# Performance work log

Measured on AMD Instinct MI355X. Metric: run time of the kernel, lower is better.

## Reference

```python
import jax, jax.numpy as jnp
import numpy as np

N_NODES = 40000


def setup_inputs() -> dict:
    key = jax.random.key(0)
    k_h, k_w, k_b, k_s, k_d = jax.random.split(key, 5)
    in_feats, out_feats, n_edges = 128, 128, 640000
    h = jax.random.normal(k_h, (N_NODES, in_feats), dtype=jnp.float32)
    # nn.Linear(in_feats, out_feats): weight [out, in], bias [out]
    W = jax.random.normal(k_w, (out_feats, in_feats), dtype=jnp.float32) * (1.0 / np.sqrt(in_feats))
    b = jax.random.normal(k_b, (out_feats,), dtype=jnp.float32) * 0.01
    src = jax.random.randint(k_s, (n_edges,), 0, N_NODES, dtype=jnp.int32)
    dst = jax.random.randint(k_d, (n_edges,), 0, N_NODES, dtype=jnp.int32)
    return {"h": h, "W": W, "b": b, "src": src, "dst": dst}


def reference(h, W, b, src, dst):
    # update_all(copy_u('h','m'), sum('m','h_N')):
    # gather messages from source nodes, segment-sum into destination nodes.
    msgs = h[src]                                              # [E, in_feats] irregular gather
    agg = jax.ops.segment_sum(msgs, dst, num_segments=N_NODES)  # [N, in_feats] scatter-add
    # Source module applies the linear to h (agg is computed but unused there);
    # we return agg as a second output so the SpMM is observable.
    out = h @ W.T + b                                          # [N, out_feats]
    return out, agg
```

## Files before the change

kernel.cpp:

```cpp
#include <hip/hip_runtime.h>

#define FEAT   128
#define RS     64
#define RSH    6
#define CAPN   64
#define NRMAX  1024
#define PART   256
#define SLOTS  32
#define SLOTSH 5
#define STR    (PART * SLOTS)

typedef short bf16x8 __attribute__((ext_vector_type(8)));
typedef float f32x4  __attribute__((ext_vector_type(4)));

__device__ __forceinline__ unsigned pack_bf16x2(float x, float y) {
    unsigned ux = __float_as_uint(x);
    ux = (ux + 0x7fffu + ((ux >> 16) & 1u)) >> 16;
    unsigned uy = __float_as_uint(y);
    uy = (uy + 0x7fffu + ((uy >> 16) & 1u)) & 0xffff0000u;
    return uy | ux;
}

__device__ __forceinline__ bf16x8 pack8(float4 a, float4 b) {
    uint4 u = make_uint4(pack_bf16x2(a.x, a.y), pack_bf16x2(a.z, a.w),
                         pack_bf16x2(b.x, b.y), pack_bf16x2(b.z, b.w));
    return __builtin_bit_cast(bf16x8, u);
}

__device__ __forceinline__ f32x4 unpack2(unsigned x, unsigned y) {
    return (f32x4){__uint_as_float(x << 16), __uint_as_float(x & 0xffff0000u),
                   __uint_as_float(y << 16), __uint_as_float(y & 0xffff0000u)};
}

__global__ __launch_bounds__(512) void fused_kernel(
    const float* __restrict__ h, const float* __restrict__ W,
    const float* __restrict__ b, const int* __restrict__ src,
    const int* __restrict__ dst, float* __restrict__ out,
    uint4* __restrict__ hb4, unsigned* __restrict__ seg, int* __restrict__ cnt,
    int n, int E, int NR)
{
    __shared__ int hist[NRMAX];

    const int bid = blockIdx.x;
    const int tid = threadIdx.x;

    if (bid < PART) {
        for (int i = tid; i < NR; i += 512) hist[i] = 0;
        __syncthreads();

        const int epb = (((E + PART - 1) / PART) + 3) & ~3;
        const int e0  = bid * epb;
        int e1 = e0 + epb; if (e1 > E) e1 = E;

        if (e0 < e1) {
            const int nq4 = (e1 - e0) >> 2;
            const int4* __restrict__ d4p = (const int4*)(dst + e0);
            const int4* __restrict__ s4p = (const int4*)(src + e0);
            const size_t sb = (size_t)bid * SLOTS;

            for (int i = tid; i < nq4; i += 512) {
                int4 d = d4p[i];
                int4 s = s4p[i];
#pragma unroll
                for (int u = 0; u < 4; ++u) {
                    int dv = (u == 0) ? d.x : (u == 1) ? d.y : (u == 2) ? d.z : d.w;
                    int sv = (u == 0) ? s.x : (u == 1) ? s.y : (u == 2) ? s.z : s.w;
                    int rid  = dv >> RSH;
                    int slot = atomicAdd(&hist[rid], 1);
                    if (slot < SLOTS)
                        seg[(size_t)rid * STR + sb + slot] =
                            (unsigned)(((dv & (RS - 1)) << 16) | (sv & 0xffff));
                }
            }
            for (int e = e0 + (nq4 << 2) + tid; e < e1; e += 512) {
                int dv = dst[e], sv = src[e];
                int rid  = dv >> RSH;
                int slot = atomicAdd(&hist[rid], 1);
                if (slot < SLOTS)
                    seg[(size_t)rid * STR + sb + slot] =
                        (unsigned)(((dv & (RS - 1)) << 16) | (sv & 0xffff));
            }
        }
        __syncthreads();

        for (int r = tid; r < NR; r += 512) {
            int c = hist[r]; if (c > SLOTS) c = SLOTS;
            cnt[(size_t)r * PART + bid] = c;
        }
        return;
    }

    const int gbid = bid - PART;
    const int w    = tid >> 6;
    const int lane = tid & 63;
    const int m    = lane & 15, quad = lane >> 4;
    const int r0g  = gbid * 128 + (w >> 1) * 32;
    const int ch   = w & 1;
    if (r0g >= n) return;

    const float4* __restrict__ h4 = (const float4*)h;
    const float4* __restrict__ W4 = (const float4*)W;

    bf16x8 af[2][4];
#pragma unroll
    for (int mt = 0; mt < 2; ++mt) {
        int gr = r0g + mt * 16 + m;
#pragma unroll
        for (int ks = 0; ks < 4; ++ks) {
            float4 a0 = h4[(size_t)gr * 32 + ks * 8 + quad * 2];
            float4 a1 = h4[(size_t)gr * 32 + ks * 8 + quad * 2 + 1];
            af[mt][ks] = pack8(a0, a1);
        }
    }

    if (ch == 0) {
#pragma unroll
        for (int mt = 0; mt < 2; ++mt) {
            int gr = r0g + mt * 16 + m;
            if (gr < n) {
#pragma unroll
                for (int ks = 0; ks < 4; ++ks)
                    hb4[(size_t)gr * 16 + ks * 4 + quad] = __builtin_bit_cast(uint4, af[mt][ks]);
            }
        }
    }

    f32x4 acc[2][4];
#pragma unroll
    for (int mt = 0; mt < 2; ++mt)
#pragma unroll
        for (int nn = 0; nn < 4; ++nn) acc[mt][nn] = (f32x4){0.f, 0.f, 0.f, 0.f};

#pragma unroll
    for (int nn = 0; nn < 4; ++nn) {
        int c = (ch * 4 + nn) * 16 + m;
#pragma unroll
        for (int ks = 0; ks < 4; ++ks) {
            float4 b0 = W4[(size_t)c * 32 + ks * 8 + quad * 2];
            float4 b1 = W4[(size_t)c * 32 + ks * 8 + quad * 2 + 1];
            bf16x8 bf = pack8(b0, b1);
#pragma unroll
            for (int mt = 0; mt < 2; ++mt)
                acc[mt][nn] = __builtin_amdgcn_mfma_f32_16x16x32_bf16(
                    af[mt][ks], bf, acc[mt][nn], 0, 0, 0);
        }
    }

#pragma unroll
    for (int nn = 0; nn < 4; ++nn) {
        int col = (ch * 4 + nn) * 16 + m;
        float bias = b[col];
#pragma unroll
        for (int mt = 0; mt < 2; ++mt)
#pragma unroll
            for (int r = 0; r < 4; ++r) {
                int gr = r0g + mt * 16 + quad * 4 + r;
                if (gr < n)
                    __builtin_nontemporal_store(acc[mt][nn][r] + bias,
                                                &out[(size_t)gr * FEAT + col]);
            }
    }
}

__global__ __launch_bounds__(512) void bin_gather_kernel(
    const uint4* __restrict__ hb4, const unsigned* __restrict__ seg,
    const int* __restrict__ cnt, float* __restrict__ agg, int n, int NR)
{
    __shared__ int            lcnt[RS];
    __shared__ int            scnt[PART];
    __shared__ unsigned short lbkt[RS * CAPN];

    const int bid = blockIdx.x;
    const int tid = threadIdx.x;

    const int base = bid * RS;
    int rsv = n - base; if (rsv > RS) rsv = RS;

    if (tid < RS) lcnt[tid] = 0;
    if (tid < PART) scnt[tid] = cnt[(size_t)bid * PART + tid];
    __syncthreads();

    const int4* __restrict__ seg4 = (const int4*)seg + (size_t)bid * (STR / 4);
#pragma unroll
    for (int wv = 0; wv < STR / 4 / 512; ++wv) {
        int j4 = wv * 512 + tid;
        int4 pv = seg4[j4];
        int s0 = j4 << 2;
#pragma unroll
        for (int u = 0; u < 4; ++u) {
            int sl = s0 + u;
            unsigned p = (u == 0) ? (unsigned)pv.x : (u == 1) ? (unsigned)pv.y
                       : (u == 2) ? (unsigned)pv.z : (unsigned)pv.w;
            if ((sl & (SLOTS - 1)) < scnt[sl >> SLOTSH]) {
                int nd = (int)(p >> 16);
                int k  = atomicAdd(&lcnt[nd], 1);
                if (k < CAPN) lbkt[(nd << 6) + k] = (unsigned short)(p & 0xffffu);
            }
        }
    }
    __syncthreads();

    const int lane = tid & 63;
    const int w    = tid >> 6;
    const int q    = lane >> 4, ql = lane & 15;
    const int nb   = w << 3;

    for (int k = 0; k < 8; k += 2) {
        const int ndA = nb + k, ndB = nb + k + 1;
        if (ndA >= rsv) break;
        const bool hasB = (ndB < rsv);
        int degA = lcnt[ndA]; degA = degA > CAPN ? CAPN : degA;
        int degB = hasB ? lcnt[ndB] : 0; degB = degB > CAPN ? CAPN : degB;
        const int dmax = degA > degB ? degA : degB;
        const int rbA = ndA << 6, rbB = ndB << 6;

        f32x4 alA0 = {0.f,0.f,0.f,0.f}, ahA0 = {0.f,0.f,0.f,0.f};
        f32x4 alA1 = {0.f,0.f,0.f,0.f}, ahA1 = {0.f,0.f,0.f,0.f};
        f32x4 alB0 = {0.f,0.f,0.f,0.f}, ahB0 = {0.f,0.f,0.f,0.f};
        f32x4 alB1 = {0.f,0.f,0.f,0.f}, ahB1 = {0.f,0.f,0.f,0.f};

        for (int t = 0; t < dmax; t += 16) {
            const int i0 = t + q, i1 = t + 4 + q, i2 = t + 8 + q, i3 = t + 12 + q;
            int eA0 = lbkt[rbA + i0], eA1 = lbkt[rbA + i1];
            int eA2 = lbkt[rbA + i2], eA3 = lbkt[rbA + i3];
            int eB0 = lbkt[rbB + i0], eB1 = lbkt[rbB + i1];
            int eB2 = lbkt[rbB + i2], eB3 = lbkt[rbB + i3];
            uint4 vA0, vA1, vA2, vA3, vB0, vB1, vB2, vB3;
            if (i0 < degA) vA0 = hb4[(size_t)eA0 * 16 + ql];
            if (i1 < degA) vA1 = hb4[(size_t)eA1 * 16 + ql];
            if (i2 < degA) vA2 = hb4[(size_t)eA2 * 16 + ql];
            if (i3 < degA) vA3 = hb4[(size_t)eA3 * 16 + ql];
            if (i0 < degB) vB0 = hb4[(size_t)eB0 * 16 + ql];
            if (i1 < degB) vB1 = hb4[(size_t)eB1 * 16 + ql];
            if (i2 < degB) vB2 = hb4[(size_t)eB2 * 16 + ql];
            if (i3 < degB) vB3 = hb4[(size_t)eB3 * 16 + ql];
            if (i0 < degA) { alA0 += unpack2(vA0.x, vA0.y); ahA0 += unpack2(vA0.z, vA0.w); }
            if (i1 < degA) { alA1 += unpack2(vA1.x, vA1.y); ahA1 += unpack2(vA1.z, vA1.w); }
            if (i2 < degA) { alA0 += unpack2(vA2.x, vA2.y); ahA0 += unpack2(vA2.z, vA2.w); }
            if (i3 < degA) { alA1 += unpack2(vA3.x, vA3.y); ahA1 += unpack2(vA3.z, vA3.w); }
            if (i0 < degB) { alB0 += unpack2(vB0.x, vB0.y); ahB0 += unpack2(vB0.z, vB0.w); }
            if (i1 < degB) { alB1 += unpack2(vB1.x, vB1.y); ahB1 += unpack2(vB1.z, vB1.w); }
            if (i2 < degB) { alB0 += unpack2(vB2.x, vB2.y); ahB0 += unpack2(vB2.z, vB2.w); }
            if (i3 < degB) { alB1 += unpack2(vB3.x, vB3.y); ahB1 += unpack2(vB3.z, vB3.w); }
        }

        alA0 += alA1; ahA0 += ahA1;
        alB0 += alB1; ahB0 += ahB1;

#pragma unroll
        for (int j = 0; j < 4; ++j) {
            alA0[j] += __shfl_down(alA0[j], 32);
            ahA0[j] += __shfl_down(ahA0[j], 32);
            alB0[j] += __shfl_down(alB0[j], 32);
            ahB0[j] += __shfl_down(ahB0[j], 32);
            alA0[j] += __shfl_down(alA0[j], 16);
            ahA0[j] += __shfl_down(ahA0[j], 16);
            alB0[j] += __shfl_down(alB0[j], 16);
            ahB0[j] += __shfl_down(ahB0[j], 16);
        }

        if (q == 0) {
            f32x4* aggv = (f32x4*)agg;
            __builtin_nontemporal_store(alA0, &aggv[(size_t)(base + ndA) * 32 + ql * 2]);
            __builtin_nontemporal_store(ahA0, &aggv[(size_t)(base + ndA) * 32 + ql * 2 + 1]);
            if (hasB) {
                __builtin_nontemporal_store(alB0, &aggv[(size_t)(base + ndB) * 32 + ql * 2]);
                __builtin_nontemporal_store(ahB0, &aggv[(size_t)(base + ndB) * 32 + ql * 2 + 1]);
            }
        }
    }
}

__global__ __launch_bounds__(256, 2) void gemm_f32_kernel(
    const float* __restrict__ h, const float* __restrict__ W,
    const float* __restrict__ b, float* __restrict__ out, int nrows)
{
    __shared__ float4 wsh[128 * 8];
    __shared__ float4 hsh[64 * 8];
    const int tid = threadIdx.x;
    const int tx  = tid & 31;
    const int ty  = tid >> 5;
    const int r0  = blockIdx.x * 64;
    const float4* __restrict__ W4 = (const float4*)W;
    const float4* __restrict__ h4 = (const float4*)h;
    float acc[8][4];
#pragma unroll
    for (int i = 0; i < 8; ++i)
#pragma unroll
        for (int j = 0; j < 4; ++j) acc[i][j] = 0.f;
    for (int p = 0; p < 4; ++p) {
        if (p) __syncthreads();
#pragma unroll
        for (int l = 0; l < 4; ++l) {
            int flat = l * 256 + tid;
            int c = flat >> 3, kc = flat & 7;
            wsh[c * 8 + (kc ^ ((c >> 2) & 7))] = W4[c * 32 + p * 8 + kc];
        }
#pragma unroll
        for (int l = 0; l < 2; ++l) {
            int flat = l * 256 + tid;
            int r = flat >> 3, kc = flat & 7;
            int gr = r0 + r;
            float4 v = make_float4(0.f, 0.f, 0.f, 0.f);
            if (gr < nrows) v = h4[(size_t)gr * 32 + p * 8 + kc];
            hsh[r * 8 + (kc ^ ((r >> 2) & 7))] = v;
        }
        __syncthreads();
#pragma unroll
        for (int kc = 0; kc < 8; ++kc) {
            float4 wv[4], hv[8];
#pragma unroll
            for (int j = 0; j < 4; ++j) wv[j] = wsh[(4 * tx + j) * 8 + (kc ^ (tx & 7))];
#pragma unroll
            for (int i = 0; i < 8; ++i) {
                int r = 8 * ty + i;
                hv[i] = hsh[r * 8 + (kc ^ ((r >> 2) & 7))];
            }
#pragma unroll
            for (int i = 0; i < 8; ++i)
#pragma unroll
                for (int j = 0; j < 4; ++j) {
                    acc[i][j] += hv[i].x * wv[j].x;
                    acc[i][j] += hv[i].y * wv[j].y;
                    acc[i][j] += hv[i].z * wv[j].z;
                    acc[i][j] += hv[i].w * wv[j].w;
                }
        }
    }
    const float4 bj = ((const float4*)b)[tx];
    float4* out4 = (float4*)out;
#pragma unroll
    for (int i = 0; i < 8; ++i) {
        int gr = r0 + 8 * ty + i;
        if (gr < nrows) {
            float4 o;
            o.x = acc[i][0] + bj.x; o.y = acc[i][1] + bj.y;
            o.z = acc[i][2] + bj.z; o.w = acc[i][3] + bj.w;
            out4[(size_t)gr * 32 + tx] = o;
        }
    }
}

__global__ __launch_bounds__(256) void scatter_add_kernel(
    const float* __restrict__ h, const int* __restrict__ src,
    const int* __restrict__ dst, float* __restrict__ agg, int E)
{
    int gid  = blockIdx.x * 256 + threadIdx.x;
    int e    = gid >> 6;
    int lane = gid & 63;
    if (e >= E) return;
    int s = src[e];
    int d = dst[e];
    const float2* hp = (const float2*)(h + (size_t)s * FEAT);
    float2 v = hp[lane];
    float* ap = agg + (size_t)d * FEAT + 2 * lane;
    unsafeAtomicAdd(ap,     v.x);
    unsafeAtomicAdd(ap + 1, v.y);
}

extern "C" void kernel_launch(void* const* d_in, const int* in_sizes, int n_in,
                              void* d_out, int out_size, void* d_ws, size_t ws_size,
                              hipStream_t stream) {
    const float* h   = (const float*)d_in[0];
    const float* W   = (const float*)d_in[1];
    const float* b   = (const float*)d_in[2];
    const int*   src = (const int*)d_in[3];
    const int*   dst = (const int*)d_in[4];

    const int n = in_sizes[0] / FEAT;
    const int E = in_sizes[3];

    float* out = (float*)d_out;
    float* agg = out + (size_t)n * FEAT;

    const int NR = (n + RS - 1) >> RSH;

    size_t hb_bytes  = (size_t)n * FEAT * 2;
    size_t seg_bytes = (size_t)NR * STR * 4;
    size_t cnt_bytes = (size_t)NR * PART * 4;
    size_t need = hb_bytes + seg_bytes + cnt_bytes;

    bool fast = (ws_size >= need) && (n > 0) && (n <= 65536) && (NR <= NRMAX);

    if (fast) {
        uint4*    hb  = (uint4*)d_ws;
        unsigned* seg = (unsigned*)((char*)d_ws + hb_bytes);
        int*      cnt = (int*)((char*)d_ws + hb_bytes + seg_bytes);

        int gemm_blocks = (n + 127) / 128;
        fused_kernel<<<dim3(PART + gemm_blocks), dim3(512), 0, stream>>>(
            h, W, b, src, dst, out, hb, seg, cnt, n, E, NR);

        bin_gather_kernel<<<dim3(NR), dim3(512), 0, stream>>>(
            hb, seg, cnt, agg, n, NR);
    } else {
        gemm_f32_kernel<<<dim3((n + 63) / 64), dim3(256), 0, stream>>>(h, W, b, out, n);
        (void)hipMemsetAsync(agg, 0, (size_t)n * FEAT * sizeof(float), stream);
        int nblocks = (int)(((long long)E * 64 + 255) / 256);
        scatter_add_kernel<<<dim3(nblocks), dim3(256), 0, stream>>>(h, src, dst, agg, E);
    }
}
```

Measured before the change: 150.9 us.

## Split bf16 feature copy into feature planes and gather per plane

The bf16 copy of h is now stored as 8 feature planes of 16 values each (32 bytes per node per plane), so each plane is 1.25 MB instead of one 10 MB table. The binning and gather stages are split into two kernels: bin_kernel writes per-range edge buckets and degrees to workspace, and plane_gather_kernel launches NR*8 blocks, each summing one plane for 64 destination nodes. The aim is to keep each plane's random-gather working set cache-resident and to raise parallelism. In exchange it adds a kernel launch, extra bucket traffic through global memory, bucket reloads per plane, and narrower 8-byte gathers.

```diff
diff --git a/kernel.cpp b/kernel.cpp
--- a/kernel.cpp
+++ b/kernel.cpp
@@ -9,6 +9,7 @@
 #define SLOTS  32
 #define SLOTSH 5
 #define STR    (PART * SLOTS)
+#define NPL    8
 
 typedef short bf16x8 __attribute__((ext_vector_type(8)));
 typedef float f32x4  __attribute__((ext_vector_type(4)));
@@ -36,7 +37,7 @@
     const float* __restrict__ h, const float* __restrict__ W,
     const float* __restrict__ b, const int* __restrict__ src,
     const int* __restrict__ dst, float* __restrict__ out,
-    uint4* __restrict__ hb4, unsigned* __restrict__ seg, int* __restrict__ cnt,
+    uint4* __restrict__ hbp4, unsigned* __restrict__ seg, int* __restrict__ cnt,
     int n, int E, int NR)
 {
     __shared__ int hist[NRMAX];
@@ -114,13 +115,17 @@
     }
 
     if (ch == 0) {
+        const int pq   = quad >> 1;
+        const int half = quad & 1;
 #pragma unroll
         for (int mt = 0; mt < 2; ++mt) {
             int gr = r0g + mt * 16 + m;
             if (gr < n) {
 #pragma unroll
-                for (int ks = 0; ks < 4; ++ks)
-                    hb4[(size_t)gr * 16 + ks * 4 + quad] = __builtin_bit_cast(uint4, af[mt][ks]);
+                for (int ks = 0; ks < 4; ++ks) {
+                    int p = ks * 2 + pq;
+                    hbp4[((size_t)p * n + gr) * 2 + half] = __builtin_bit_cast(uint4, af[mt][ks]);
+                }
             }
         }
     }
@@ -162,19 +167,18 @@
     }
 }
 
-__global__ __launch_bounds__(512) void bin_gather_kernel(
-    const uint4* __restrict__ hb4, const unsigned* __restrict__ seg,
-    const int* __restrict__ cnt, float* __restrict__ agg, int n, int NR)
+__global__ __launch_bounds__(512) void bin_kernel(
+    const unsigned* __restrict__ seg, const int* __restrict__ cnt,
+    unsigned short* __restrict__ bucket, unsigned char* __restrict__ counts,
+    int n, int NR)
 {
     __shared__ int            lcnt[RS];
     __shared__ int            scnt[PART];
     __shared__ unsigned short lbkt[RS * CAPN];
 
-    const int bid = blockIdx.x;
-    const int tid = threadIdx.x;
-
+    const int bid  = blockIdx.x;
+    const int tid  = threadIdx.x;
     const int base = bid * RS;
-    int rsv = n - base; if (rsv > RS) rsv = RS;
 
     if (tid < RS) lcnt[tid] = 0;
     if (tid < PART) scnt[tid] = cnt[(size_t)bid * PART + tid];
@@ -200,74 +204,68 @@
     }
     __syncthreads();
 
+    uint4* bg = (uint4*)(bucket + (size_t)bid * RS * CAPN);
+    bg[tid] = ((const uint4*)lbkt)[tid];
+    if (tid < RS) {
+        int c = lcnt[tid]; if (c > CAPN) c = CAPN;
+        counts[base + tid] = (unsigned char)c;
+    }
+}
+
+__global__ __launch_bounds__(512) void plane_gather_kernel(
+    const uint4* __restrict__ hbp4, const unsigned short* __restrict__ bucket,
+    const unsigned char* __restrict__ counts, float* __restrict__ agg, int n, int NR)
+{
+    __shared__ unsigned short sbkt[RS * CAPN];
+    __shared__ int            sdeg[RS];
+
+    const int bid   = blockIdx.x;
+    const int p     = bid & (NPL - 1);
+    const int range = bid >> 3;
+    const int tid   = threadIdx.x;
+    const int base  = range * RS;
+    int rsv = n - base; if (rsv > RS) rsv = RS;
+
+    ((uint4*)sbkt)[tid] = ((const uint4*)(bucket + (size_t)range * RS * CAPN))[tid];
+    if (tid < RS) sdeg[tid] = counts[base + tid];
+    __syncthreads();
+
     const int lane = tid & 63;
     const int w    = tid >> 6;
-    const int q    = lane >> 4, ql = lane & 15;
-    const int nb   = w << 3;
-
-    for (int k = 0; k < 8; k += 2) {
-        const int ndA = nb + k, ndB = nb + k + 1;
-        if (ndA >= rsv) break;
-        const bool hasB = (ndB < rsv);
-        int degA = lcnt[ndA]; degA = degA > CAPN ? CAPN : degA;
-        int degB = hasB ? lcnt[ndB] : 0; degB = degB > CAPN ? CAPN : degB;
-        const int dmax = degA > degB ? degA : degB;
-        const int rbA = ndA << 6, rbB = ndB << 6;
-
-        f32x4 alA0 = {0.f,0.f,0.f,0.f}, ahA0 = {0.f,0.f,0.f,0.f};
-        f32x4 alA1 = {0.f,0.f,0.f,0.f}, ahA1 = {0.f,0.f,0.f,0.f};
-        f32x4 alB0 = {0.f,0.f,0.f,0.f}, ahB0 = {0.f,0.f,0.f,0.f};
-        f32x4 alB1 = {0.f,0.f,0.f,0.f}, ahB1 = {0.f,0.f,0.f,0.f};
-
-        for (int t = 0; t < dmax; t += 16) {
-            const int i0 = t + q, i1 = t + 4 + q, i2 = t + 8 + q, i3 = t + 12 + q;
-            int eA0 = lbkt[rbA + i0], eA1 = lbkt[rbA + i1];
-            int eA2 = lbkt[rbA + i2], eA3 = lbkt[rbA + i3];
-            int eB0 = lbkt[rbB + i0], eB1 = lbkt[rbB + i1];
-            int eB2 = lbkt[rbB + i2], eB3 = lbkt[rbB + i3];
-            uint4 vA0, vA1, vA2, vA3, vB0, vB1, vB2, vB3;
-            if (i0 < degA) vA0 = hb4[(size_t)eA0 * 16 + ql];
-            if (i1 < degA) vA1 = hb4[(size_t)eA1 * 16 + ql];
-            if (i2 < degA) vA2 = hb4[(size_t)eA2 * 16 + ql];
-            if (i3 < degA) vA3 = hb4[(size_t)eA3 * 16 + ql];
-            if (i0 < degB) vB0 = hb4[(size_t)eB0 * 16 + ql];
-            if (i1 < degB) vB1 = hb4[(size_t)eB1 * 16 + ql];
-            if (i2 < degB) vB2 = hb4[(size_t)eB2 * 16 + ql];
-            if (i3 < degB) vB3 = hb4[(size_t)eB3 * 16 + ql];
-            if (i0 < degA) { alA0 += unpack2(vA0.x, vA0.y); ahA0 += unpack2(vA0.z, vA0.w); }
-            if (i1 < degA) { alA1 += unpack2(vA1.x, vA1.y); ahA1 += unpack2(vA1.z, vA1.w); }
-            if (i2 < degA) { alA0 += unpack2(vA2.x, vA2.y); ahA0 += unpack2(vA2.z, vA2.w); }
-            if (i3 < degA) { alA1 += unpack2(vA3.x, vA3.y); ahA1 += unpack2(vA3.z, vA3.w); }
-            if (i0 < degB) { alB0 += unpack2(vB0.x, vB0.y); ahB0 += unpack2(vB0.z, vB0.w); }
-            if (i1 < degB) { alB1 += unpack2(vB1.x, vB1.y); ahB1 += unpack2(vB1.z, vB1.w); }
-            if (i2 < degB) { alB0 += unpack2(vB2.x, vB2.y); ahB0 += unpack2(vB2.z, vB2.w); }
-            if (i3 < degB) { alB1 += unpack2(vB3.x, vB3.y); ahB1 += unpack2(vB3.z, vB3.w); }
-        }
-
-        alA0 += alA1; ahA0 += ahA1;
-        alB0 += alB1; ahB0 += ahB1;
+    const int e    = lane >> 2;
+    const int f    = lane & 3;
+    const uint2* __restrict__ hp2 = (const uint2*)hbp4 + (size_t)p * n * 4;
+    f32x4* aggv = (f32x4*)agg;
+
+    for (int k = 0; k < 8; ++k) {
+        int nd = (w << 3) + k;
+        if (nd >= rsv) break;
+        int deg = sdeg[nd]; if (deg > CAPN) deg = CAPN;
+        const int rowb = nd << 6;
+
+        f32x4 a0 = {0.f,0.f,0.f,0.f}, a1 = {0.f,0.f,0.f,0.f};
+        for (int t = 0; t < deg; t += 32) {
+            int i0 = t + e, i1 = t + 16 + e;
+            int e0 = sbkt[rowb + i0];
+            int e1 = sbkt[rowb + i1];
+            uint2 v0, v1;
+            if (i0 < deg) v0 = hp2[((size_t)e0 << 2) + f];
+            if (i1 < deg) v1 = hp2[((size_t)e1 << 2) + f];
+            if (i0 < deg) a0 += unpack2(v0.x, v0.y);
+            if (i1 < deg) a1 += unpack2(v1.x, v1.y);
+        }
+        a0 += a1;
 
 #pragma unroll
         for (int j = 0; j < 4; ++j) {
-            alA0[j] += __shfl_down(alA0[j], 32);
-            ahA0[j] += __shfl_down(ahA0[j], 32);
-            alB0[j] += __shfl_down(alB0[j], 32);
-            ahB0[j] += __shfl_down(ahB0[j], 32);
-            alA0[j] += __shfl_down(alA0[j], 16);
-            ahA0[j] += __shfl_down(ahA0[j], 16);
-            alB0[j] += __shfl_down(alB0[j], 16);
-            ahB0[j] += __shfl_down(ahB0[j], 16);
-        }
-
-        if (q == 0) {
-            f32x4* aggv = (f32x4*)agg;
-            __builtin_nontemporal_store(alA0, &aggv[(size_t)(base + ndA) * 32 + ql * 2]);
-            __builtin_nontemporal_store(ahA0, &aggv[(size_t)(base + ndA) * 32 + ql * 2 + 1]);
-            if (hasB) {
-                __builtin_nontemporal_store(alB0, &aggv[(size_t)(base + ndB) * 32 + ql * 2]);
-                __builtin_nontemporal_store(ahB0, &aggv[(size_t)(base + ndB) * 32 + ql * 2 + 1]);
-            }
-        }
+            a0[j] += __shfl_down(a0[j], 32);
+            a0[j] += __shfl_down(a0[j], 16);
+            a0[j] += __shfl_down(a0[j], 8);
+            a0[j] += __shfl_down(a0[j], 4);
+        }
+
+        if (lane < 4)
+            __builtin_nontemporal_store(a0, &aggv[(size_t)(base + nd) * 32 + p * 4 + lane]);
     }
 }
 
@@ -375,24 +373,32 @@
 
     const int NR = (n + RS - 1) >> RSH;
 
-    size_t hb_bytes  = (size_t)n * FEAT * 2;
+    size_t hbp_bytes = (size_t)n * FEAT * 2;
     size_t seg_bytes = (size_t)NR * STR * 4;
     size_t cnt_bytes = (size_t)NR * PART * 4;
-    size_t need = hb_bytes + seg_bytes + cnt_bytes;
+    size_t bkt_bytes = (size_t)NR * RS * CAPN * 2;
+    size_t cts_bytes = (size_t)NR * RS;
+    size_t need = hbp_bytes + seg_bytes + cnt_bytes + bkt_bytes + cts_bytes;
 
     bool fast = (ws_size >= need) && (n > 0) && (n <= 65536) && (NR <= NRMAX);
 
     if (fast) {
-        uint4*    hb  = (uint4*)d_ws;
-        unsigned* seg = (unsigned*)((char*)d_ws + hb_bytes);
-        int*      cnt = (int*)((char*)d_ws + hb_bytes + seg_bytes);
+        char* w0 = (char*)d_ws;
+        uint4*          hbp    = (uint4*)w0;                       w0 += hbp_bytes;
+        unsigned*       seg    = (unsigned*)w0;                    w0 += seg_bytes;
+        int*            cnt    = (int*)w0;                         w0 += cnt_bytes;
+        unsigned short* bucket = (unsigned short*)w0;              w0 += bkt_bytes;
+        unsigned char*  counts = (unsigned char*)w0;
 
         int gemm_blocks = (n + 127) / 128;
         fused_kernel<<<dim3(PART + gemm_blocks), dim3(512), 0, stream>>>(
-            h, W, b, src, dst, out, hb, seg, cnt, n, E, NR);
-
-        bin_gather_kernel<<<dim3(NR), dim3(512), 0, stream>>>(
-            hb, seg, cnt, agg, n, NR);
+            h, W, b, src, dst, out, hbp, seg, cnt, n, E, NR);
+
+        bin_kernel<<<dim3(NR), dim3(512), 0, stream>>>(
+            seg, cnt, bucket, counts, n, NR);
+
+        plane_gather_kernel<<<dim3(NR * NPL), dim3(512), 0, stream>>>(
+            hbp, bucket, counts, agg, n, NR);
     } else {
         gemm_f32_kernel<<<dim3((n + 63) / 64), dim3(256), 0, stream>>>(h, W, b, out, n);
         (void)hipMemsetAsync(agg, 0, (size_t)n * FEAT * sizeof(float), stream);
```

Measured after the change: 180.1 us. 1.19x slower.
